# Kernel optimization log

Hardware: AMD Instinct MI355X
Metric: run time of the kernel (lower is better)

The kernel has to match this reference:

```python
import jax, jax.numpy as jnp
import numpy as np
import math

PHI = (1 + math.sqrt(5)) / 2
TABLE_SIZE = 4096
TWO_PI = 2.0 * math.pi
_ang = np.arange(TABLE_SIZE, dtype=np.float32) * (TWO_PI / TABLE_SIZE)
SIN_T = jnp.asarray(np.sin(_ang))
COS_T = jnp.asarray(np.cos(_ang))


def lookup_sin_cos(theta):
    """LUT sin/cos with linear interpolation over a 4096-entry table on [0, 2pi)."""
    pos = (theta / TWO_PI % 1.0) * TABLE_SIZE
    i0f = jnp.floor(pos)
    frac = pos - i0f
    i0 = i0f.astype(jnp.int32) % TABLE_SIZE
    i1 = (i0 + 1) % TABLE_SIZE
    s = SIN_T[i0] * (1.0 - frac) + SIN_T[i1] * frac
    c = COS_T[i0] * (1.0 - frac) + COS_T[i1] * frac
    return s, c


def setup_inputs() -> dict:
    key = jax.random.key(0)
    ks = jax.random.split(key, 8)
    B, S, D, H = 2, 2048, 1024, 16
    dh = D // H
    return {
        "x": jax.random.normal(ks[0], (B, S, D), dtype=jnp.float32),
        "w_q": jax.random.normal(ks[1], (H, dh), dtype=jnp.float32) * 0.02,
        "b_q": jnp.zeros((H, dh), jnp.float32),
        "phi_q": jnp.full((H, dh), PHI, jnp.float32),
        "w_k": jax.random.normal(ks[2], (H, dh), dtype=jnp.float32) * 0.02,
        "b_k": jnp.zeros((H, dh), jnp.float32),
        "phi_k": jnp.full((H, dh), PHI, jnp.float32),
        "w_v": jax.random.normal(ks[3], (H, dh), dtype=jnp.float32) * 0.02,
        "b_v": jnp.zeros((H, dh), jnp.float32),
        "w_out": jax.random.normal(ks[4], (D,), dtype=jnp.float32) * 0.02,
        "b_out": jnp.zeros((D,), jnp.float32),
    }


def reference(x, w_q, b_q, phi_q, w_k, b_k, phi_k, w_v, b_v, w_out, b_out):
    B, S, D = x.shape
    H, dh = w_q.shape
    scale = math.sqrt(2 * dh)
    t = jnp.arange(S, dtype=x.dtype).reshape(1, S, 1, 1)
    xh = x.reshape(B, S, H, dh)

    theta_q = xh / (1.0 + jnp.abs(w_q)) + b_q + t * phi_q
    sin_q, cos_q = lookup_sin_cos(theta_q)
    Q = jnp.concatenate([cos_q, sin_q], axis=-1)  # (B,S,H,2dh)

    theta_k = xh / (1.0 + jnp.abs(w_k)) + b_k + t * phi_k
    sin_k, cos_k = lookup_sin_cos(theta_k)
    K = jnp.concatenate([cos_k, sin_k], axis=-1)  # (B,S,H,2dh)

    theta_v = xh / (1.0 + jnp.abs(w_v)) + b_v
    sin_v, cos_v = lookup_sin_cos(theta_v)
    V = cos_v + sin_v  # (B,S,H,dh)

    scores = jnp.einsum('bqhd,bkhd->bhqk', Q, K) / scale
    causal = jnp.triu(jnp.ones((S, S), dtype=bool), k=1)
    scores = jnp.where(causal, -jnp.inf, scores)
    attn = jax.nn.softmax(scores, axis=-1)
    out = jnp.einsum('bhqk,bkhd->bqhd', attn, V).reshape(B, S, D)

    theta_out = out / (1.0 + jnp.abs(w_out)) + b_out
    sin_o, cos_o = lookup_sin_cos(theta_out)
    return cos_o + sin_o
```

## Files before the change

### kernel.cpp

```cpp
#include <hip/hip_runtime.h>
#include <hip/hip_bf16.h>
#include <math.h>

#define BB 2
#define SS 2048
#define HH 16
#define DH 64
#define DQK 128
#define DD (HH*DH)
#define QSCALE 0.08838834764831845f

typedef _Float16 half8_t __attribute__((ext_vector_type(8)));
typedef _Float16 half4_t __attribute__((ext_vector_type(4)));
typedef float f32x4_t __attribute__((ext_vector_type(4)));
typedef float f32x4v __attribute__((ext_vector_type(4)));

__device__ __forceinline__ void fsincos(float th, float* sn, float* cs) {
  float rev = th * 0.15915494309189535f;
  rev -= floorf(rev);
  float ang = rev * 6.283185307179586f;
  *sn = __sinf(ang);
  *cs = __cosf(ang);
}

__device__ __forceinline__ void dma16(const void* g, void* l) {
  __builtin_amdgcn_global_load_lds(
      (const __attribute__((address_space(1))) unsigned int*)g,
      (__attribute__((address_space(3))) unsigned int*)l, 16, 0, 0);
}

__global__ __launch_bounds__(256) void gen_qkv(
    const float* __restrict__ x,
    const float* __restrict__ wq, const float* __restrict__ bq,
    const float* __restrict__ phq,
    const float* __restrict__ wk, const float* __restrict__ bk,
    const float* __restrict__ phk,
    const float* __restrict__ wv, const float* __restrict__ bv,
    _Float16* __restrict__ Qd, _Float16* __restrict__ Kd, _Float16* __restrict__ Vtd)
{
  int stile = blockIdx.x & 31;
  int bh    = blockIdx.x >> 5;
  int b = bh >> 4, h = bh & 15;
  int t = threadIdx.x;
  int sl = t >> 2;
  int dq = (t & 3) << 4;
  int s  = stile * 64 + sl;

  __shared__ _Float16 Vl[64 * 65];

  const float* xr = x + (((size_t)b * SS + s) * HH + h) * DH + dq;
  float xv[16];
#pragma unroll
  for (int i = 0; i < 4; i++)
    *(f32x4v*)(&xv[i * 4]) = *(const f32x4v*)(xr + i * 4);

  float tv = (float)s;
  _Float16 qc[16], qs[16], kc[16], ks[16];
#pragma unroll
  for (int i = 0; i < 16; i++) {
    int d = dq + i;
    int hd = h * DH + d;
    {
      float th = xv[i] / (1.f + fabsf(wq[hd])) + bq[hd] + tv * phq[hd];
      float sn, cs; fsincos(th, &sn, &cs);
      qc[i] = (_Float16)(cs * QSCALE);
      qs[i] = (_Float16)(sn * QSCALE);
    }
    {
      float th = xv[i] / (1.f + fabsf(wk[hd])) + bk[hd] + tv * phk[hd];
      float sn, cs; fsincos(th, &sn, &cs);
      kc[i] = (_Float16)cs;
      ks[i] = (_Float16)sn;
    }
    {
      float th = xv[i] / (1.f + fabsf(wv[hd])) + bv[hd];
      float sn, cs; fsincos(th, &sn, &cs);
      Vl[d * 65 + sl] = (_Float16)(cs + sn);
    }
  }
  size_t qbase = ((size_t)bh * SS + s) * DQK;
#pragma unroll
  for (int i = 0; i < 2; i++) {
    *(half8_t*)(Qd + qbase + dq + i * 8)      = *(half8_t*)(&qc[i * 8]);
    *(half8_t*)(Qd + qbase + DH + dq + i * 8) = *(half8_t*)(&qs[i * 8]);
  }
  {
    size_t ktb = ((size_t)bh * 32 + stile) * 8192;
    int fo0 = (t & 3) * 2;
    *(half8_t*)(Kd + ktb + ((size_t)(fo0    ) * 64 + sl) * 8) = *(half8_t*)(&kc[0]);
    *(half8_t*)(Kd + ktb + ((size_t)(fo0 + 1) * 64 + sl) * 8) = *(half8_t*)(&kc[8]);
    *(half8_t*)(Kd + ktb + ((size_t)(fo0 + 8) * 64 + sl) * 8) = *(half8_t*)(&ks[0]);
    *(half8_t*)(Kd + ktb + ((size_t)(fo0 + 9) * 64 + sl) * 8) = *(half8_t*)(&ks[8]);
  }
  __syncthreads();
#pragma unroll
  for (int i = 0; i < 2; i++) {
    int u = t * 2 + i;
    int dv = u & 63, ku = u >> 6;
    _Float16 tmp[8];
#pragma unroll
    for (int jj = 0; jj < 8; jj++) tmp[jj] = Vl[dv * 65 + ku * 8 + jj];
    *(half8_t*)(Vtd + (((size_t)bh * 32 + stile) * 8 + ku) * 512 + dv * 8) =
        *(half8_t*)tmp;
  }
}

__global__ __launch_bounds__(256) void flash_attn(
    const _Float16* __restrict__ Qd, const _Float16* __restrict__ Kd,
    const _Float16* __restrict__ Vtd,
    const float* __restrict__ wout, const float* __restrict__ bout,
    float* __restrict__ out)
{
  int j  = blockIdx.x >> 5;
  int bh = blockIdx.x & 31;
  int wave = threadIdx.x >> 6;
  int lane = threadIdx.x & 63;
  int lm = lane & 15, lq = lane >> 4;
  int qh = wave >> 1;
  int kh = wave & 1;

  __shared__ __align__(16) _Float16 KV[2][12288];
  __shared__ __align__(16) float Of[64 * 68];
  __shared__ __align__(16) float Lf[64];

  const _Float16* Kg = Kd + (size_t)bh * 32 * 8192;
  const _Float16* Vg = Vtd + (size_t)bh * 32 * 4096;

  for (int phase = 0; phase < 2; ++phase) {
    int qt = phase == 0 ? (31 - j) : j;
    int nch = qt + 1;
    int q0 = qt * 64;

    __syncthreads();

    const _Float16* Qb = Qd + ((size_t)bh * SS + q0 + qh * 32) * DQK;
    half8_t aq[2][4];
#pragma unroll
    for (int qtl = 0; qtl < 2; qtl++)
#pragma unroll
      for (int c = 0; c < 4; c++)
        aq[qtl][c] = *(const half8_t*)(Qb + (qtl * 16 + lm) * DQK + c * 32 + lq * 8);

    f32x4_t o[4][2];
    float l[2] = {0.f, 0.f};
#pragma unroll
    for (int dt = 0; dt < 4; dt++)
#pragma unroll
      for (int qtl = 0; qtl < 2; qtl++) o[dt][qtl] = (f32x4_t){0.f, 0.f, 0.f, 0.f};

    {
#pragma unroll
      for (int i = 0; i < 4; i++)
        dma16(Kg + (size_t)(wave * 4 + i) * 512 + lane * 8, &KV[0][(wave * 4 + i) * 512]);
#pragma unroll
      for (int i = 0; i < 2; i++)
        dma16(Vg + (size_t)(wave * 2 + i) * 512 + lane * 8, &KV[0][8192 + (wave * 2 + i) * 512]);
    }

    for (int kt = 0; kt < nch; ++kt) {
      int bf = kt & 1;
      __syncthreads();
      if (kt + 1 < nch) {
        int nb = (kt + 1) & 1;
        const _Float16* gK = Kg + (size_t)(kt + 1) * 8192;
        const _Float16* gV = Vg + (size_t)(kt + 1) * 4096;
#pragma unroll
        for (int i = 0; i < 4; i++)
          dma16(gK + (size_t)(wave * 4 + i) * 512 + lane * 8, &KV[nb][(wave * 4 + i) * 512]);
#pragma unroll
        for (int i = 0; i < 2; i++)
          dma16(gV + (size_t)(wave * 2 + i) * 512 + lane * 8, &KV[nb][8192 + (wave * 2 + i) * 512]);
      }

      const _Float16* lK = &KV[bf][0];
      const _Float16* lV = &KV[bf][8192];
      int k0 = kt * 64;

      f32x4_t cST[2][2];
      cST[0][0] = cST[0][1] = cST[1][0] = cST[1][1] = (f32x4_t){0.f, 0.f, 0.f, 0.f};
#pragma unroll
      for (int c = 0; c < 4; c++) {
        half8_t k0f = *(const half8_t*)(lK + ((size_t)(c * 4 + lq) * 64 + kh * 32 + lm) * 8);
        half8_t k1f = *(const half8_t*)(lK + ((size_t)(c * 4 + lq) * 64 + kh * 32 + 16 + lm) * 8);
        cST[0][0] = __builtin_amdgcn_mfma_f32_16x16x32_f16(k0f, aq[0][c], cST[0][0], 0, 0, 0);
        cST[0][1] = __builtin_amdgcn_mfma_f32_16x16x32_f16(k0f, aq[1][c], cST[0][1], 0, 0, 0);
        cST[1][0] = __builtin_amdgcn_mfma_f32_16x16x32_f16(k1f, aq[0][c], cST[1][0], 0, 0, 0);
        cST[1][1] = __builtin_amdgcn_mfma_f32_16x16x32_f16(k1f, aq[1][c], cST[1][1], 0, 0, 0);
      }

      bool maskit = (kt == nch - 1);
      half4_t pb[2][2];
#pragma unroll
      for (int ktl = 0; ktl < 2; ktl++)
#pragma unroll
        for (int qtl = 0; qtl < 2; qtl++) {
          float pf[4];
#pragma unroll
          for (int r = 0; r < 4; r++) {
            float sv = cST[ktl][qtl][r] - 8.f;
            if (maskit) {
              int key  = k0 + kh * 32 + ktl * 16 + lq * 4 + r;
              int qrow = q0 + qh * 32 + qtl * 16 + lm;
              if (key > qrow) sv = -1e30f;
            }
            pf[r] = __expf(sv);
            l[qtl] += pf[r];
          }
          pb[ktl][qtl] = (half4_t){(_Float16)pf[0], (_Float16)pf[1],
                                   (_Float16)pf[2], (_Float16)pf[3]};
        }

#pragma unroll
      for (int dt = 0; dt < 4; dt++)
#pragma unroll
        for (int kg = 0; kg < 2; kg++) {
          half4_t vf = *(const half4_t*)(lV +
              ((size_t)(kh * 4 + kg * 2 + (lq >> 1)) * 64 + dt * 16 + lm) * 8 + (lq & 1) * 4);
          o[dt][0] = __builtin_amdgcn_mfma_f32_16x16x16f16(vf, pb[kg][0], o[dt][0], 0, 0, 0);
          o[dt][1] = __builtin_amdgcn_mfma_f32_16x16x16f16(vf, pb[kg][1], o[dt][1], 0, 0, 0);
        }
    }

#pragma unroll
    for (int qtl = 0; qtl < 2; qtl++) {
      l[qtl] += __shfl_xor(l[qtl], 16);
      l[qtl] += __shfl_xor(l[qtl], 32);
    }

    __syncthreads();
    if (kh == 1) {
#pragma unroll
      for (int qtl = 0; qtl < 2; qtl++) {
        int row = qh * 32 + qtl * 16 + lm;
#pragma unroll
        for (int dt = 0; dt < 4; dt++)
#pragma unroll
          for (int r = 0; r < 4; r++)
            Of[row * 68 + dt * 16 + lq * 4 + r] = o[dt][qtl][r];
        if (lq == 0) Lf[row] = l[qtl];
      }
    }
    __syncthreads();
    if (kh == 0) {
#pragma unroll
      for (int qtl = 0; qtl < 2; qtl++) {
        int row = qh * 32 + qtl * 16 + lm;
        float rl = 1.f / (l[qtl] + Lf[row]);
#pragma unroll
        for (int dt = 0; dt < 4; dt++)
#pragma unroll
          for (int r = 0; r < 4; r++) {
            int idx = row * 68 + dt * 16 + lq * 4 + r;
            Of[idx] = (o[dt][qtl][r] + Of[idx]) * rl;
          }
      }
    }
    __syncthreads();
    {
      int b = bh >> 4, hh = bh & 15;
      int dcol = hh * DH + lane;
      float iw = 1.f / (1.f + fabsf(wout[dcol]));
      float bo = bout[dcol];
#pragma unroll
      for (int rr = 0; rr < 16; rr++) {
        int row = wave * 16 + rr;
        float th = Of[row * 68 + lane] * iw + bo;
        float sn, cs; fsincos(th, &sn, &cs);
        out[((size_t)b * SS + q0 + row) * DD + dcol] = cs + sn;
      }
    }
  }
}

extern "C" void kernel_launch(void* const* d_in, const int* in_sizes, int n_in,
                              void* d_out, int out_size, void* d_ws, size_t ws_size,
                              hipStream_t stream) {
  (void)in_sizes; (void)n_in; (void)out_size; (void)ws_size;
  const float* x   = (const float*)d_in[0];
  const float* wq  = (const float*)d_in[1];
  const float* bq  = (const float*)d_in[2];
  const float* phq = (const float*)d_in[3];
  const float* wk  = (const float*)d_in[4];
  const float* bk  = (const float*)d_in[5];
  const float* phk = (const float*)d_in[6];
  const float* wv  = (const float*)d_in[7];
  const float* bv  = (const float*)d_in[8];
  const float* wo  = (const float*)d_in[9];
  const float* bo  = (const float*)d_in[10];

  _Float16* Qd  = (_Float16*)d_ws;
  _Float16* Kd  = Qd + (size_t)BB * HH * SS * DQK;
  _Float16* Vtd = Kd + (size_t)BB * HH * SS * DQK;

  gen_qkv<<<BB * HH * (SS / 64), 256, 0, stream>>>(
      x, wq, bq, phq, wk, bk, phk, wv, bv, Qd, Kd, Vtd);
  flash_attn<<<BB * HH * 16, 256, 0, stream>>>(
      Qd, Kd, Vtd, wo, bo, (float*)d_out);
}
```

Measured before the change: 146.4 us.

## Compute Q inside attention kernel, use exp2 with folded scale, reuse LDS

Q generation moves from the pre-pass kernel into the flash-attention kernel. Each wave computes its Q fragments straight from x in registers, so the Q buffer is no longer written to and read back from global memory. The softmax scale and log2(e) are folded into the Q scaling (QS2) and the bias (EBIAS), which lets the exponent use exp2 directly. The output-reduction scratch reuses the idle K/V LDS buffer, the initial K/V DMA is issued before the Q math so the two overlap, and launch bounds request 3 blocks per CU. In exchange, Q sin/cos is computed redundantly by the key-half waves, and register pressure is higher.

```diff
diff --git a/kernel.cpp b/kernel.cpp
--- a/kernel.cpp
+++ b/kernel.cpp
@@ -8,7 +8,8 @@
 #define DH 64
 #define DQK 128
 #define DD (HH*DH)
-#define QSCALE 0.08838834764831845f
+#define QS2   0.12751758f
+#define EBIAS 11.5415605f
 
 typedef _Float16 half8_t __attribute__((ext_vector_type(8)));
 typedef _Float16 half4_t __attribute__((ext_vector_type(4)));
@@ -29,14 +30,12 @@
       (__attribute__((address_space(3))) unsigned int*)l, 16, 0, 0);
 }
 
-__global__ __launch_bounds__(256) void gen_qkv(
+__global__ __launch_bounds__(256) void gen_kv(
     const float* __restrict__ x,
-    const float* __restrict__ wq, const float* __restrict__ bq,
-    const float* __restrict__ phq,
     const float* __restrict__ wk, const float* __restrict__ bk,
     const float* __restrict__ phk,
     const float* __restrict__ wv, const float* __restrict__ bv,
-    _Float16* __restrict__ Qd, _Float16* __restrict__ Kd, _Float16* __restrict__ Vtd)
+    _Float16* __restrict__ Kd, _Float16* __restrict__ Vtd)
 {
   int stile = blockIdx.x & 31;
   int bh    = blockIdx.x >> 5;
@@ -55,17 +54,11 @@
     *(f32x4v*)(&xv[i * 4]) = *(const f32x4v*)(xr + i * 4);
 
   float tv = (float)s;
-  _Float16 qc[16], qs[16], kc[16], ks[16];
+  _Float16 kc[16], ks[16];
 #pragma unroll
   for (int i = 0; i < 16; i++) {
     int d = dq + i;
     int hd = h * DH + d;
-    {
-      float th = xv[i] / (1.f + fabsf(wq[hd])) + bq[hd] + tv * phq[hd];
-      float sn, cs; fsincos(th, &sn, &cs);
-      qc[i] = (_Float16)(cs * QSCALE);
-      qs[i] = (_Float16)(sn * QSCALE);
-    }
     {
       float th = xv[i] / (1.f + fabsf(wk[hd])) + bk[hd] + tv * phk[hd];
       float sn, cs; fsincos(th, &sn, &cs);
@@ -77,12 +70,6 @@
       float sn, cs; fsincos(th, &sn, &cs);
       Vl[d * 65 + sl] = (_Float16)(cs + sn);
     }
-  }
-  size_t qbase = ((size_t)bh * SS + s) * DQK;
-#pragma unroll
-  for (int i = 0; i < 2; i++) {
-    *(half8_t*)(Qd + qbase + dq + i * 8)      = *(half8_t*)(&qc[i * 8]);
-    *(half8_t*)(Qd + qbase + DH + dq + i * 8) = *(half8_t*)(&qs[i * 8]);
   }
   {
     size_t ktb = ((size_t)bh * 32 + stile) * 8192;
@@ -105,14 +92,17 @@
   }
 }
 
-__global__ __launch_bounds__(256) void flash_attn(
-    const _Float16* __restrict__ Qd, const _Float16* __restrict__ Kd,
-    const _Float16* __restrict__ Vtd,
+__global__ __launch_bounds__(256, 3) void flash_attn(
+    const float* __restrict__ x,
+    const float* __restrict__ wq, const float* __restrict__ bq,
+    const float* __restrict__ phq,
+    const _Float16* __restrict__ Kd, const _Float16* __restrict__ Vtd,
     const float* __restrict__ wout, const float* __restrict__ bout,
     float* __restrict__ out)
 {
   int j  = blockIdx.x >> 5;
   int bh = blockIdx.x & 31;
+  int b  = bh >> 4, hh = bh & 15;
   int wave = threadIdx.x >> 6;
   int lane = threadIdx.x & 63;
   int lm = lane & 15, lq = lane >> 4;
@@ -120,8 +110,6 @@
   int kh = wave & 1;
 
   __shared__ __align__(16) _Float16 KV[2][12288];
-  __shared__ __align__(16) float Of[64 * 68];
-  __shared__ __align__(16) float Lf[64];
 
   const _Float16* Kg = Kd + (size_t)bh * 32 * 8192;
   const _Float16* Vg = Vtd + (size_t)bh * 32 * 4096;
@@ -133,13 +121,41 @@
 
     __syncthreads();
 
-    const _Float16* Qb = Qd + ((size_t)bh * SS + q0 + qh * 32) * DQK;
+    {
+#pragma unroll
+      for (int i = 0; i < 4; i++)
+        dma16(Kg + (size_t)(wave * 4 + i) * 512 + lane * 8, &KV[0][(wave * 4 + i) * 512]);
+#pragma unroll
+      for (int i = 0; i < 2; i++)
+        dma16(Vg + (size_t)(wave * 2 + i) * 512 + lane * 8, &KV[0][8192 + (wave * 2 + i) * 512]);
+    }
+
     half8_t aq[2][4];
 #pragma unroll
-    for (int qtl = 0; qtl < 2; qtl++)
-#pragma unroll
-      for (int c = 0; c < 4; c++)
-        aq[qtl][c] = *(const half8_t*)(Qb + (qtl * 16 + lm) * DQK + c * 32 + lq * 8);
+    for (int qtl = 0; qtl < 2; qtl++) {
+      int row = q0 + qh * 32 + qtl * 16 + lm;
+      const float* xr = x + (((size_t)b * SS + row) * HH + hh) * DH;
+      float xv[16];
+      *(f32x4v*)(&xv[0])  = *(const f32x4v*)(xr + lq * 8);
+      *(f32x4v*)(&xv[4])  = *(const f32x4v*)(xr + lq * 8 + 4);
+      *(f32x4v*)(&xv[8])  = *(const f32x4v*)(xr + 32 + lq * 8);
+      *(f32x4v*)(&xv[12]) = *(const f32x4v*)(xr + 32 + lq * 8 + 4);
+      float trow = (float)row;
+      _Float16 qc[16], qs[16];
+#pragma unroll
+      for (int jj = 0; jj < 16; jj++) {
+        int d  = (jj < 8 ? lq * 8 + jj : 32 + lq * 8 + (jj - 8));
+        int hd = hh * DH + d;
+        float th = xv[jj] / (1.f + fabsf(wq[hd])) + bq[hd] + trow * phq[hd];
+        float sn, cs; fsincos(th, &sn, &cs);
+        qc[jj] = (_Float16)(cs * QS2);
+        qs[jj] = (_Float16)(sn * QS2);
+      }
+      aq[qtl][0] = *(half8_t*)(&qc[0]);
+      aq[qtl][1] = *(half8_t*)(&qc[8]);
+      aq[qtl][2] = *(half8_t*)(&qs[0]);
+      aq[qtl][3] = *(half8_t*)(&qs[8]);
+    }
 
     f32x4_t o[4][2];
     float l[2] = {0.f, 0.f};
@@ -147,15 +163,6 @@
     for (int dt = 0; dt < 4; dt++)
 #pragma unroll
       for (int qtl = 0; qtl < 2; qtl++) o[dt][qtl] = (f32x4_t){0.f, 0.f, 0.f, 0.f};
-
-    {
-#pragma unroll
-      for (int i = 0; i < 4; i++)
-        dma16(Kg + (size_t)(wave * 4 + i) * 512 + lane * 8, &KV[0][(wave * 4 + i) * 512]);
-#pragma unroll
-      for (int i = 0; i < 2; i++)
-        dma16(Vg + (size_t)(wave * 2 + i) * 512 + lane * 8, &KV[0][8192 + (wave * 2 + i) * 512]);
-    }
 
     for (int kt = 0; kt < nch; ++kt) {
       int bf = kt & 1;
@@ -197,13 +204,13 @@
           float pf[4];
 #pragma unroll
           for (int r = 0; r < 4; r++) {
-            float sv = cST[ktl][qtl][r] - 8.f;
+            float sv = cST[ktl][qtl][r] - EBIAS;
             if (maskit) {
               int key  = k0 + kh * 32 + ktl * 16 + lq * 4 + r;
               int qrow = q0 + qh * 32 + qtl * 16 + lm;
               if (key > qrow) sv = -1e30f;
             }
-            pf[r] = __expf(sv);
+            pf[r] = __builtin_exp2f(sv);
             l[qtl] += pf[r];
           }
           pb[ktl][qtl] = (half4_t){(_Float16)pf[0], (_Float16)pf[1],
@@ -227,6 +234,9 @@
       l[qtl] += __shfl_xor(l[qtl], 32);
     }
 
+    int sc = nch & 1;
+    float* Of = (float*)&KV[sc][0];
+    float* Lf = Of + 64 * 68;
     __syncthreads();
     if (kh == 1) {
 #pragma unroll
@@ -257,7 +267,6 @@
     }
     __syncthreads();
     {
-      int b = bh >> 4, hh = bh & 15;
       int dcol = hh * DH + lane;
       float iw = 1.f / (1.f + fabsf(wout[dcol]));
       float bo = bout[dcol];
@@ -288,12 +297,11 @@
   const float* wo  = (const float*)d_in[9];
   const float* bo  = (const float*)d_in[10];
 
-  _Float16* Qd  = (_Float16*)d_ws;
-  _Float16* Kd  = Qd + (size_t)BB * HH * SS * DQK;
+  _Float16* Kd  = (_Float16*)d_ws;
   _Float16* Vtd = Kd + (size_t)BB * HH * SS * DQK;
 
-  gen_qkv<<<BB * HH * (SS / 64), 256, 0, stream>>>(
-      x, wq, bq, phq, wk, bk, phk, wv, bv, Qd, Kd, Vtd);
+  gen_kv<<<BB * HH * (SS / 64), 256, 0, stream>>>(
+      x, wk, bk, phk, wv, bv, Kd, Vtd);
   flash_attn<<<BB * HH * 16, 256, 0, stream>>>(
-      Qd, Kd, Vtd, wo, bo, (float*)d_out);
-}
+      x, wq, bq, phq, Kd, Vtd, wo, bo, (float*)d_out);
+}
```

Measured after the change: 160.9 us. 10.0% more time.
